# Kernel tuning notes

Hardware: AMD Instinct MI355X
Metric: run time of the kernel (lower is better)

The kernel has to match this reference:

```python
import jax, jax.numpy as jnp
import numpy as np

GC = 128      # mem_dim
HEADS = 4     # gc / att_head_dim
HD = 32       # att_head_dim


def _dwconv(x, w, b, pad):
    # depthwise conv, NCHW, weight OIHW with I=1, groups=GC
    y = jax.lax.conv_general_dilated(
        x, w, window_strides=(1, 1),
        padding=((pad[0], pad[0]), (pad[1], pad[1])),
        feature_group_count=GC,
        dimension_numbers=('NCHW', 'OIHW', 'NCHW'))
    return y + b[None, :, None, None]


def setup_inputs() -> dict:
    key = jax.random.key(0)
    ks = jax.random.split(key, 5)
    x = jax.random.normal(ks[0], (32, 512, 56, 56), dtype=jnp.float32)
    w_dw1 = jax.random.normal(ks[1], (GC, 1, 3, 3), dtype=jnp.float32) * 0.1
    b_dw1 = jnp.zeros((GC,), jnp.float32)
    w_dw2 = jax.random.normal(ks[2], (GC, 1, 7, 7), dtype=jnp.float32) * 0.05
    b_dw2 = jnp.zeros((GC,), jnp.float32)
    w_qk = jax.random.normal(ks[3], (2 * GC, GC, 1, 1), dtype=jnp.float32) * (1.0 / np.sqrt(GC))
    b_qk = jnp.zeros((2 * GC,), jnp.float32)
    return {"x": x, "w_dw1": w_dw1, "b_dw1": b_dw1, "w_dw2": w_dw2,
            "b_dw2": b_dw2, "w_qk": w_qk, "b_qk": b_qk}


def reference(x, w_dw1, b_dw1, w_dw2, b_dw2, w_qk, b_qk):
    B, C, H, W = x.shape
    HW = H * W
    # grasp_memory + asymmetric_decouple (split along channels)
    m0 = C - 3 * GC
    mem = x[:, :m0]
    feat_att = x[:, m0:m0 + GC]
    feat_conv1 = x[:, m0 + GC:m0 + 2 * GC]
    feat_conv2 = x[:, m0 + 2 * GC:]
    feat_conv1 = _dwconv(feat_conv1, w_dw1, b_dw1, (1, 1))
    feat_conv2 = _dwconv(feat_conv2, w_dw2, b_dw2, (3, 3))
    # 1x1 conv qk -> [B, 2*GC, H, W]
    qk = jnp.einsum('bchw,oc->bohw', feat_att, w_qk[:, :, 0, 0]) + b_qk[None, :, None, None]
    qk = qk.reshape(B, 2 * GC, HW)
    q = qk[:, :GC].reshape(B, HEADS, HD, HW).transpose(0, 1, 3, 2)   # [B,h,HW,d]
    k = qk[:, GC:].reshape(B, HEADS, HD, HW).transpose(0, 1, 3, 2)
    v = feat_att.reshape(B, HEADS, HD, HW).transpose(0, 1, 3, 2)
    q = jax.nn.elu(q) + 1.0
    k = jax.nn.elu(k) + 1.0
    kmean = k.mean(axis=2, keepdims=True)                            # [B,h,1,d]
    z = 1.0 / (jnp.einsum('bhnd,bhmd->bhnm', q, kmean) + 1e-6)       # [B,h,HW,1]
    kv = jnp.einsum('bhnd,bhne->bhde', k, v) / HW                    # [B,h,d,d]
    att = jnp.einsum('bhnd,bhde->bhne', q, kv) * z                   # [B,h,HW,d]
    feat_att_out = att.transpose(0, 1, 3, 2).reshape(B, GC, H, W)
    feats = jnp.concatenate([feat_att_out, feat_conv1, feat_conv2], axis=1)
    return (mem, feats)
```

## Files before the change

kernel.cpp:

```cpp
#include <hip/hip_runtime.h>
#include <hip/hip_bf16.h>

#define Bn   32
#define Cn   512
#define GCn  128
#define HWn  3136
#define M0   128

#define Q_ELEMS  (Bn*GCn*HWn)
#define KV_ELEMS (Bn*4*32*32)
#define KS_ELEMS (Bn*4*32)

typedef __attribute__((ext_vector_type(8))) short bf16x8;
typedef __attribute__((ext_vector_type(4))) float f32x4;
typedef __attribute__((ext_vector_type(4))) float nf4;
typedef __attribute__((ext_vector_type(2))) float nf2;

__device__ __forceinline__ float bf2f(unsigned short u) {
    union { unsigned int i; float f; } v; v.i = ((unsigned int)u) << 16; return v.f;
}
__device__ __forceinline__ unsigned short f2bf(float f) {
    union { __hip_bfloat16 h; unsigned short u; } v; v.h = __float2bfloat16(f); return v.u;
}
__device__ __forceinline__ float act_elu1(float v) {
    return v > 0.0f ? v + 1.0f : __expf(v);
}
__device__ __forceinline__ void nt_store4(float* p, float a, float b, float c, float d) {
    nf4 v; v.x = a; v.y = b; v.z = c; v.w = d;
    __builtin_nontemporal_store(v, (nf4*)p);
}
__device__ __forceinline__ void nt_store2(float* p, float a, float b) {
    nf2 v; v.x = a; v.y = b;
    __builtin_nontemporal_store(v, (nf2*)p);
}

__global__ __launch_bounds__(256) void k_pre(
    const float* __restrict__ w_qk, unsigned short* __restrict__ wfrag) {
    int idx = blockIdx.x * 256 + threadIdx.x;
    int j  = idx & 7;
    int l  = (idx >> 3) & 63;
    int ks = (idx >> 9) & 3;
    int mt = idx >> 11;
    int o = mt * 16 + (l & 15);
    int c = ks * 32 + (l >> 4) * 8 + j;
    wfrag[idx] = f2bf(w_qk[o * 128 + c]);
}

__device__ __forceinline__ void main_dev(
    const float* __restrict__ x, const unsigned short* __restrict__ wfrag,
    const float* __restrict__ b_qk,
    unsigned short* __restrict__ q_ws, float* __restrict__ kv_g,
    float* __restrict__ ks_g,
    unsigned short* Xn, unsigned short* Klds, int nt, int b) {

    unsigned short* Qlds = Xn;

    const int t  = threadIdx.x;
    const int n0 = nt * 64;
    const float* xa = x + ((long long)(b * Cn + M0)) * HWn;

    {
        const int cpair = t & 63;
        const int seg   = t >> 6;
        const float* s0 = xa + (long long)(2 * cpair) * HWn + n0 + seg * 16;
        const float* s1 = s0 + HWn;
        #pragma unroll
        for (int u = 0; u < 4; ++u) {
            float4 a  = *(const float4*)(s0 + 4 * u);
            float4 b2 = *(const float4*)(s1 + 4 * u);
            const float av[4] = {a.x, a.y, a.z, a.w};
            const float bv[4] = {b2.x, b2.y, b2.z, b2.w};
            #pragma unroll
            for (int j = 0; j < 4; ++j) {
                const int n = seg * 16 + 4 * u + j;
                unsigned int pk = (unsigned int)f2bf(av[j]) |
                                  ((unsigned int)f2bf(bv[j]) << 16);
                *(unsigned int*)(Xn + n * 144 + 2 * cpair) = pk;
            }
        }
    }
    __syncthreads();

    const int w = t >> 6, l = t & 63, nn = l & 15, q = l >> 4;
    f32x4 acc[4][4] = {};

    #pragma unroll
    for (int ks = 0; ks < 4; ++ks) {
        bf16x8 bq[4];
        #pragma unroll
        for (int in = 0; in < 4; ++in)
            bq[in] = *(const bf16x8*)(Xn + (in * 16 + nn) * 144 + ks * 32 + q * 8);
        #pragma unroll
        for (int im = 0; im < 4; ++im) {
            const int mt = 4 * w + im;
            bf16x8 aq = *(const bf16x8*)(wfrag + ((mt * 4 + ks) * 64 + l) * 8);
            #pragma unroll
            for (int in = 0; in < 4; ++in)
                acc[im][in] = __builtin_amdgcn_mfma_f32_16x16x32_bf16(aq, bq[in], acc[im][in], 0, 0, 0);
        }
    }

    if (w >= 2) {
        #pragma unroll
        for (int im = 0; im < 4; ++im) {
            const int obase = w * 64 + im * 16 + q * 4;
            float4 bias4 = *(const float4*)(b_qk + obase);
            const int krow = obase - 128;
            #pragma unroll
            for (int r = 0; r < 4; ++r) {
                const float bias = ((const float*)&bias4)[r];
                #pragma unroll
                for (int in = 0; in < 4; ++in)
                    Klds[(krow + r) * 72 + in * 16 + nn] = f2bf(act_elu1(acc[im][in][r] + bias));
            }
        }
    }
    __syncthreads();

    if (w < 2) {
        #pragma unroll
        for (int im = 0; im < 4; ++im) {
            const int obase = w * 64 + im * 16 + q * 4;
            float4 bias4 = *(const float4*)(b_qk + obase);
            #pragma unroll
            for (int r = 0; r < 4; ++r) {
                const float bias = ((const float*)&bias4)[r];
                #pragma unroll
                for (int in = 0; in < 4; ++in)
                    Qlds[(obase + r) * 72 + in * 16 + nn] = f2bf(act_elu1(acc[im][in][r] + bias));
            }
        }
    }

    {
        const int h = w;
        f32x4 akv[2][2] = {};
        float ksl0 = 0.0f, ksl1 = 0.0f;
        #pragma unroll
        for (int kt = 0; kt < 2; ++kt) {
            bf16x8 af0 = *(const bf16x8*)(Klds + (h * 32 + nn) * 72 + kt * 32 + q * 8);
            bf16x8 af1 = *(const bf16x8*)(Klds + (h * 32 + 16 + nn) * 72 + kt * 32 + q * 8);
            {
                const unsigned short* a0 = (const unsigned short*)&af0;
                const unsigned short* a1 = (const unsigned short*)&af1;
                #pragma unroll
                for (int j = 0; j < 8; ++j) { ksl0 += bf2f(a0[j]); ksl1 += bf2f(a1[j]); }
            }
            #pragma unroll
            for (int vt = 0; vt < 2; ++vt) {
                const float* vsrc = xa + (long long)(h * 32 + vt * 16 + nn) * HWn + n0 + kt * 32 + q * 8;
                float4 v0 = *(const float4*)(vsrc);
                float4 v1 = *(const float4*)(vsrc + 4);
                short tb[8];
                tb[0] = (short)f2bf(v0.x); tb[1] = (short)f2bf(v0.y);
                tb[2] = (short)f2bf(v0.z); tb[3] = (short)f2bf(v0.w);
                tb[4] = (short)f2bf(v1.x); tb[5] = (short)f2bf(v1.y);
                tb[6] = (short)f2bf(v1.z); tb[7] = (short)f2bf(v1.w);
                bf16x8 bv = *(bf16x8*)tb;
                akv[0][vt] = __builtin_amdgcn_mfma_f32_16x16x32_bf16(af0, bv, akv[0][vt], 0, 0, 0);
                akv[1][vt] = __builtin_amdgcn_mfma_f32_16x16x32_bf16(af1, bv, akv[1][vt], 0, 0, 0);
            }
        }
        const int bh = b * 4 + h;
        #pragma unroll
        for (int mt = 0; mt < 2; ++mt)
            #pragma unroll
            for (int vt = 0; vt < 2; ++vt)
                #pragma unroll
                for (int r = 0; r < 4; ++r)
                    atomicAdd(&kv_g[(bh << 10) + (mt * 16 + q * 4 + r) * 32 + vt * 16 + nn],
                              akv[mt][vt][r]);
        float s0 = ksl0; s0 += __shfl_xor(s0, 16, 64); s0 += __shfl_xor(s0, 32, 64);
        float s1 = ksl1; s1 += __shfl_xor(s1, 16, 64); s1 += __shfl_xor(s1, 32, 64);
        if (l < 16) {
            atomicAdd(&ks_g[bh * 32 + nn],      s0);
            atomicAdd(&ks_g[bh * 32 + 16 + nn], s1);
        }
    }
    __syncthreads();

    {
        const int row = t >> 1, hf = t & 1;
        const unsigned short* sp = Qlds + row * 72 + hf * 32;
        unsigned short* dp = q_ws + ((long long)(b * GCn + row)) * HWn + n0 + hf * 32;
        #pragma unroll
        for (int p = 0; p < 4; ++p)
            *(bf16x8*)(dp + p * 8) = *(const bf16x8*)(sp + p * 8);
    }
}

__global__ __launch_bounds__(256) void k_maincopy(
    const float* __restrict__ x, const unsigned short* __restrict__ wfrag,
    const float* __restrict__ b_qk,
    unsigned short* __restrict__ q_ws, float* __restrict__ kv_g,
    float* __restrict__ ks_g, float* __restrict__ mem_out) {

    __shared__ __align__(16) unsigned char smem[36864];
    const int bid = blockIdx.x;
    if (bid < 1568) {
        main_dev(x, wfrag, b_qk, q_ws, kv_g, ks_g,
                 (unsigned short*)smem, (unsigned short*)(smem + 18432),
                 bid % 49, bid / 49);
    } else {
        const int r = bid - 1568;
        for (int i4 = r * 256 + (int)threadIdx.x; i4 < 3211264; i4 += 2048 * 256) {
            int b  = i4 / 100352;
            int rr = i4 - b * 100352;
            nf4 v = __builtin_nontemporal_load(((const nf4*)x) + (long long)b * 401408 + rr);
            __builtin_nontemporal_store(v, ((nf4*)mem_out) + i4);
        }
    }
}

__device__ __forceinline__ void att_dev(
    const unsigned short* __restrict__ q_ws, const float* __restrict__ kv_g,
    const float* __restrict__ ks_g, float* __restrict__ feats,
    float* kvl, float* kml, int gx, int h, int b) {

    const int t = threadIdx.x;
    const int bh = b * 4 + h;
    const float inv = 1.0f / 3136.0f;
    #pragma unroll
    for (int p = 0; p < 4; ++p) kvl[t + p * 256] = kv_g[(bh << 10) + t + p * 256] * inv;
    if (t < 32) kml[t] = ks_g[bh * 32 + t] * inv;
    __syncthreads();

    const int n2 = gx * 256 + t;
    if (n2 >= 1568) return;
    const unsigned short* qp = q_ws + ((long long)(b * GCn + h * 32)) * HWn + n2 * 2;
    float a0[32], a1[32];
    float z0 = 1e-6f, z1 = 1e-6f;
    #pragma unroll
    for (int e = 0; e < 32; ++e) { a0[e] = 0.f; a1[e] = 0.f; }
    #pragma unroll 4
    for (int d = 0; d < 32; ++d) {
        const unsigned int qq = *(const unsigned int*)(qp + (long long)d * HWn);
        const float q0 = bf2f((unsigned short)qq);
        const float q1 = bf2f((unsigned short)(qq >> 16));
        z0 = __builtin_fmaf(q0, kml[d], z0);
        z1 = __builtin_fmaf(q1, kml[d], z1);
        #pragma unroll
        for (int e = 0; e < 32; ++e) {
            const float kv = kvl[d * 32 + e];
            a0[e] = __builtin_fmaf(q0, kv, a0[e]);
            a1[e] = __builtin_fmaf(q1, kv, a1[e]);
        }
    }
    z0 = 1.f / z0; z1 = 1.f / z1;
    float* op = feats + ((long long)(b * 384 + h * 32)) * HWn + n2 * 2;
    #pragma unroll
    for (int e = 0; e < 32; ++e)
        nt_store2(op + (long long)e * HWn, a0[e] * z0, a1[e] * z1);
}

template<int KS, int PAD, int CIN>
__device__ __forceinline__ void dwconv2_dev(
    const float* __restrict__ x, const float* __restrict__ wg,
    const float* __restrict__ bg, float* __restrict__ feats,
    float* P, int cp, int b) {

    const int t = threadIdx.x;
    constexpr int ROWS = 56 + 2 * PAD;
    constexpr int PL = ROWS * 64;
    const int c0 = cp * 2;
    const float4 z4 = make_float4(0.f, 0.f, 0.f, 0.f);

    for (int i = t; i < 2 * ROWS * 16; i += 256) {
        const int ch  = (i >= ROWS * 16) ? 1 : 0;
        const int r   = i - ch * ROWS * 16;
        const int row = r >> 4, m = r & 15;
        const int y   = row - PAD;
        float4 v = z4;
        if (m >= 1 && m <= 14 && y >= 0 && y < 56)
            v = *(const float4*)(x + ((long long)(b * Cn + CIN + c0 + ch)) * HWn + y * 56 + (m - 1) * 4);
        *(float4*)(P + ch * PL + row * 64 + ((m ^ (row & 7)) << 2)) = v;
    }
    __syncthreads();

    for (int item = t; item < 392; item += 256) {
        const int ch = (item >= 196) ? 1 : 0;
        const int r  = item - ch * 196;
        const int ri = r / 7, m = r - ri * 7;
        const int y0 = ri * 2;
        const int xo = m * 8;
        const float* wp = wg + (c0 + ch) * KS * KS;
        const float bias = bg[c0 + ch];
        const float* Pc = P + ch * PL;
        float* op = feats + ((long long)(b * 384 + (CIN - 128) + c0 + ch)) * HWn;

        float a0[8], a1[8];
        #pragma unroll
        for (int j = 0; j < 8; ++j) { a0[j] = bias; a1[j] = bias; }
        #pragma unroll
        for (int dy = 0; dy <= KS; ++dy) {
            const int row = y0 + dy;
            float rr[16];
            #pragma unroll
            for (int u = 0; u < 4; ++u) {
                const int ck = ((xo >> 2) + u) ^ (row & 7);
                *(float4*)(rr + 4 * u) = *(const float4*)(Pc + row * 64 + ck * 4);
            }
            if (dy < KS) {
                #pragma unroll
                for (int dx = 0; dx < KS; ++dx) {
                    const float wv = wp[dy * KS + dx];
                    #pragma unroll
                    for (int j = 0; j < 8; ++j)
                        a0[j] = __builtin_fmaf(wv, rr[j + dx + 4 - PAD], a0[j]);
                }
            }
            if (dy >= 1) {
                #pragma unroll
                for (int dx = 0; dx < KS; ++dx) {
                    const float wv = wp[(dy - 1) * KS + dx];
                    #pragma unroll
                    for (int j = 0; j < 8; ++j)
                        a1[j] = __builtin_fmaf(wv, rr[j + dx + 4 - PAD], a1[j]);
                }
            }
        }
        nt_store4(op + y0 * 56 + xo,           a0[0], a0[1], a0[2], a0[3]);
        nt_store4(op + y0 * 56 + xo + 4,       a0[4], a0[5], a0[6], a0[7]);
        nt_store4(op + (y0 + 1) * 56 + xo,     a1[0], a1[1], a1[2], a1[3]);
        nt_store4(op + (y0 + 1) * 56 + xo + 4, a1[4], a1[5], a1[6], a1[7]);
    }
}

__global__ __launch_bounds__(256) void k_post2(
    const float* __restrict__ x,
    const unsigned short* __restrict__ q_ws, const float* __restrict__ kv_g,
    const float* __restrict__ ks_g,
    const float* __restrict__ w_dw1, const float* __restrict__ b_dw1,
    const float* __restrict__ w_dw2, const float* __restrict__ b_dw2,
    float* __restrict__ feats) {

    __shared__ __align__(16) float smem[2 * 62 * 64];
    const int bid = blockIdx.x;

    if (bid < 2048) {
        dwconv2_dev<7, 3, 384>(x, w_dw2, b_dw2, feats, smem, bid & 63, bid >> 6);
    } else if (bid < 4096) {
        const int r = bid - 2048;
        dwconv2_dev<3, 1, 256>(x, w_dw1, b_dw1, feats, smem, r & 63, r >> 6);
    } else {
        const int r = bid - 4096;
        const int b = r / 28, rem = r % 28;
        att_dev(q_ws, kv_g, ks_g, feats, smem, smem + 1024, rem % 7, rem / 7, b);
    }
}

extern "C" void kernel_launch(void* const* d_in, const int* in_sizes, int n_in,
                              void* d_out, int out_size, void* d_ws, size_t ws_size,
                              hipStream_t stream) {
    const float* x     = (const float*)d_in[0];
    const float* w_dw1 = (const float*)d_in[1];
    const float* b_dw1 = (const float*)d_in[2];
    const float* w_dw2 = (const float*)d_in[3];
    const float* b_dw2 = (const float*)d_in[4];
    const float* w_qk  = (const float*)d_in[5];
    const float* b_qk  = (const float*)d_in[6];
    float* out = (float*)d_out;

    unsigned short* q_ws = (unsigned short*)d_ws;
    float* kv_g = (float*)(q_ws + (long long)Q_ELEMS);
    float* ks_g = kv_g + KV_ELEMS;
    unsigned short* wfrag = (unsigned short*)(ks_g + KS_ELEMS);

    float* mem_out = out;
    float* feats   = out + (long long)Bn * GCn * HWn;

    hipMemsetAsync(kv_g, 0, (KV_ELEMS + KS_ELEMS) * sizeof(float), stream);
    k_pre     <<<128, 256, 0, stream>>>(w_qk, wfrag);
    k_maincopy<<<3616, 256, 0, stream>>>(x, wfrag, b_qk, q_ws, kv_g, ks_g, mem_out);
    k_post2   <<<4992, 256, 0, stream>>>(x, q_ws, kv_g, ks_g,
                                         w_dw1, b_dw1, w_dw2, b_dw2, feats);
}
```

Baseline: 425.2 us.

## Split fused main/copy kernel and run attention blocks first in post kernel

New measurement: 433.5 us. No clear change (+2.0%).

```diff
diff --git a/kernel.cpp b/kernel.cpp
--- a/kernel.cpp
+++ b/kernel.cpp
@@ -46,16 +46,19 @@
     wfrag[idx] = f2bf(w_qk[o * 128 + c]);
 }
 
-__device__ __forceinline__ void main_dev(
+__global__ __launch_bounds__(256) void k_main(
     const float* __restrict__ x, const unsigned short* __restrict__ wfrag,
     const float* __restrict__ b_qk,
     unsigned short* __restrict__ q_ws, float* __restrict__ kv_g,
-    float* __restrict__ ks_g,
-    unsigned short* Xn, unsigned short* Klds, int nt, int b) {
-
+    float* __restrict__ ks_g) {
+
+    __shared__ __align__(16) unsigned char smem[36864];
+    unsigned short* Xn   = (unsigned short*)smem;
+    unsigned short* Klds = (unsigned short*)(smem + 18432);
     unsigned short* Qlds = Xn;
 
     const int t  = threadIdx.x;
+    const int nt = blockIdx.x % 49, b = blockIdx.x / 49;
     const int n0 = nt * 64;
     const float* xa = x + ((long long)(b * Cn + M0)) * HWn;
 
@@ -189,26 +192,13 @@
     }
 }
 
-__global__ __launch_bounds__(256) void k_maincopy(
-    const float* __restrict__ x, const unsigned short* __restrict__ wfrag,
-    const float* __restrict__ b_qk,
-    unsigned short* __restrict__ q_ws, float* __restrict__ kv_g,
-    float* __restrict__ ks_g, float* __restrict__ mem_out) {
-
-    __shared__ __align__(16) unsigned char smem[36864];
-    const int bid = blockIdx.x;
-    if (bid < 1568) {
-        main_dev(x, wfrag, b_qk, q_ws, kv_g, ks_g,
-                 (unsigned short*)smem, (unsigned short*)(smem + 18432),
-                 bid % 49, bid / 49);
-    } else {
-        const int r = bid - 1568;
-        for (int i4 = r * 256 + (int)threadIdx.x; i4 < 3211264; i4 += 2048 * 256) {
-            int b  = i4 / 100352;
-            int rr = i4 - b * 100352;
-            nf4 v = __builtin_nontemporal_load(((const nf4*)x) + (long long)b * 401408 + rr);
-            __builtin_nontemporal_store(v, ((nf4*)mem_out) + i4);
-        }
+__global__ __launch_bounds__(256) void k_copy(
+    const float* __restrict__ x, float* __restrict__ mem_out) {
+    for (int i4 = blockIdx.x * 256 + (int)threadIdx.x; i4 < 3211264; i4 += 2048 * 256) {
+        int b  = i4 / 100352;
+        int rr = i4 - b * 100352;
+        nf4 v = __builtin_nontemporal_load(((const nf4*)x) + (long long)b * 401408 + rr);
+        __builtin_nontemporal_store(v, ((nf4*)mem_out) + i4);
     }
 }
 
@@ -337,15 +327,15 @@
     __shared__ __align__(16) float smem[2 * 62 * 64];
     const int bid = blockIdx.x;
 
-    if (bid < 2048) {
-        dwconv2_dev<7, 3, 384>(x, w_dw2, b_dw2, feats, smem, bid & 63, bid >> 6);
-    } else if (bid < 4096) {
-        const int r = bid - 2048;
+    if (bid < 896) {
+        const int b = bid / 28, rem = bid % 28;
+        att_dev(q_ws, kv_g, ks_g, feats, smem, smem + 1024, rem % 7, rem / 7, b);
+    } else if (bid < 2944) {
+        const int r = bid - 896;
+        dwconv2_dev<7, 3, 384>(x, w_dw2, b_dw2, feats, smem, r & 63, r >> 6);
+    } else {
+        const int r = bid - 2944;
         dwconv2_dev<3, 1, 256>(x, w_dw1, b_dw1, feats, smem, r & 63, r >> 6);
-    } else {
-        const int r = bid - 4096;
-        const int b = r / 28, rem = r % 28;
-        att_dev(q_ws, kv_g, ks_g, feats, smem, smem + 1024, rem % 7, rem / 7, b);
     }
 }
 
@@ -370,8 +360,9 @@
     float* feats   = out + (long long)Bn * GCn * HWn;
 
     hipMemsetAsync(kv_g, 0, (KV_ELEMS + KS_ELEMS) * sizeof(float), stream);
-    k_pre     <<<128, 256, 0, stream>>>(w_qk, wfrag);
-    k_maincopy<<<3616, 256, 0, stream>>>(x, wfrag, b_qk, q_ws, kv_g, ks_g, mem_out);
-    k_post2   <<<4992, 256, 0, stream>>>(x, q_ws, kv_g, ks_g,
-                                         w_dw1, b_dw1, w_dw2, b_dw2, feats);
-}
+    k_pre  <<<128, 256, 0, stream>>>(w_qk, wfrag);
+    k_main <<<1568, 256, 0, stream>>>(x, wfrag, b_qk, q_ws, kv_g, ks_g);
+    k_copy <<<2048, 256, 0, stream>>>(x, mem_out);
+    k_post2<<<4992, 256, 0, stream>>>(x, q_ws, kv_g, ks_g,
+                                      w_dw1, b_dw1, w_dw2, b_dw2, feats);
+}
```
